# Optimization experiments

Measured on AMD Instinct MI355X. Metric: run time of the kernel, lower is better.

## Reference

```python
import jax, jax.numpy as jnp
import numpy as np

N, NV, NE = 256, 8192, 128


def setup_inputs() -> dict:
    key = jax.random.key(0)
    k1, k2, k3, k4 = jax.random.split(key, 4)
    return {
        "vertices": jax.random.normal(k1, (N, NV, NE), dtype=jnp.float32),
        "query": jax.random.normal(k2, (NE,), dtype=jnp.float32) * 0.003,
        "W_logit": jax.random.normal(k3, (NE,), dtype=jnp.float32) * (1.0 / np.sqrt(NE)),
        "b_logit": jnp.zeros((), dtype=jnp.float32),
        "W_reduce": jax.random.normal(k4, (NE, NE), dtype=jnp.float32) * (1.0 / np.sqrt(NE)),
        "b_reduce": jnp.zeros((NE,), dtype=jnp.float32),
        "temp": jnp.ones((), dtype=jnp.float32),
    }


def reference(vertices, query, W_logit, b_logit, W_reduce, b_reduce, temp):
    # vertices: [N, nV, nE]; query broadcasts as the single pooling query (nQ=1).
    # Additive tanh attention logits: fc_logit(tanh(context + query)) -> [N, nV]
    logits = jnp.tanh(vertices + query) @ W_logit + b_logit  # [N, nV]
    probs = jax.nn.softmax(logits / temp, axis=-1)            # softmax over vertices
    pooled = jnp.einsum("nv,nve->ne", probs, vertices)        # bmm(probs, memory)
    heads = jax.nn.leaky_relu(pooled)                          # default slope 0.01
    out = heads @ W_reduce.T + b_reduce                        # fc_reduceheads
    return out[:, None, :]  # [N, 1, nE]
```

## Files before the change

### kernel.cpp

```cpp
#include <hip/hip_runtime.h>
#include <math.h>

#define NN      256
#define NVV     8192
#define NEE     128
#define THREADS 1024
#define WAVES   (THREADS / 64)
#define SLICES  2
#define V_PER_BLOCK (NVV / SLICES)
#define GROUPS_PER_BLOCK (WAVES * 2)
#define V_PER_GROUP (V_PER_BLOCK / GROUPS_PER_BLOCK)

__global__ __launch_bounds__(THREADS, 2) void agp_main_kernel(
    const float* __restrict__ vertices,
    const float* __restrict__ query,
    const float* __restrict__ W_logit,
    const float* __restrict__ temp_p,
    float* __restrict__ pacc,
    float* __restrict__ pl)
{
    const int bid   = blockIdx.x;
    const int n     = bid >> 1;
    const int slice = bid & 1;
    const int tid   = threadIdx.x;
    const int wave  = tid >> 6;
    const int lane  = tid & 63;
    const int half  = lane >> 5;
    const int li    = lane & 31;
    const int e0    = li << 2;
    const int gid   = (wave << 1) | half;

    const float invT   = 1.0f / temp_p[0];
    const float ESCALE = invT * 1.4426950408889634f;
    const float C2L2E  = 2.8853900817779268f;

    const float4 q4  = *reinterpret_cast<const float4*>(query   + e0);
    const float4 wl4 = *reinterpret_cast<const float4*>(W_logit + e0);
    const float qc0 = q4.x * C2L2E, qc1 = q4.y * C2L2E;
    const float qc2 = q4.z * C2L2E, qc3 = q4.w * C2L2E;
    const float swl = wl4.x + wl4.y + wl4.z + wl4.w;

    const float* p = vertices
        + ((size_t)n * NVV + (size_t)slice * V_PER_BLOCK + gid) * NEE + e0;

    float a0 = 0.f, a1 = 0.f, a2 = 0.f, a3 = 0.f;
    float l  = 0.f;

    #pragma unroll 4
    for (int it = 0; it < V_PER_GROUP; ++it, p += GROUPS_PER_BLOCK * NEE) {
        const float4 x = *reinterpret_cast<const float4*>(p);

        float s2;
        s2 =      wl4.x * __builtin_amdgcn_rcpf(__builtin_amdgcn_exp2f(fmaf(x.x, C2L2E, qc0)) + 1.0f);
        s2 = fmaf(wl4.y,  __builtin_amdgcn_rcpf(__builtin_amdgcn_exp2f(fmaf(x.y, C2L2E, qc1)) + 1.0f), s2);
        s2 = fmaf(wl4.z,  __builtin_amdgcn_rcpf(__builtin_amdgcn_exp2f(fmaf(x.z, C2L2E, qc2)) + 1.0f), s2);
        s2 = fmaf(wl4.w,  __builtin_amdgcn_rcpf(__builtin_amdgcn_exp2f(fmaf(x.w, C2L2E, qc3)) + 1.0f), s2);
        float s = fmaf(-2.0f, s2, swl);

        s += __shfl_xor(s, 1);
        s += __shfl_xor(s, 2);
        s += __shfl_xor(s, 4);
        s += __shfl_xor(s, 8);
        s += __shfl_xor(s, 16);

        const float eb = __builtin_amdgcn_exp2f(s * ESCALE);
        l += eb;
        a0 = fmaf(eb, x.x, a0);
        a1 = fmaf(eb, x.y, a1);
        a2 = fmaf(eb, x.z, a2);
        a3 = fmaf(eb, x.w, a3);
    }

    __shared__ float sm_l[GROUPS_PER_BLOCK];
    __shared__ float sm_acc[GROUPS_PER_BLOCK][NEE];

    *reinterpret_cast<float4*>(&sm_acc[gid][e0]) = make_float4(a0, a1, a2, a3);
    if (li == 0) sm_l[gid] = l;
    __syncthreads();

    if (tid < NEE) {
        float L = 0.f, P = 0.f;
        #pragma unroll
        for (int g = 0; g < GROUPS_PER_BLOCK; ++g) {
            L += sm_l[g];
            P += sm_acc[g][tid];
        }
        pacc[(size_t)bid * NEE + tid] = P;
        if (tid == 0) pl[bid] = L;
    }
}

__global__ __launch_bounds__(NEE, 8) void agp_combine_kernel(
    const float* __restrict__ pacc,
    const float* __restrict__ pl,
    const float* __restrict__ W_reduce,
    const float* __restrict__ b_reduce,
    float* __restrict__ out)
{
    const int n   = blockIdx.x;
    const int tid = threadIdx.x;

    __shared__ float sm_heads[NEE];

    const float L = pl[n * SLICES + 0] + pl[n * SLICES + 1];
    float P = pacc[(size_t)(n * SLICES + 0) * NEE + tid]
            + pacc[(size_t)(n * SLICES + 1) * NEE + tid];
    float pooled = P / L;
    sm_heads[tid] = (pooled > 0.0f) ? pooled : 0.01f * pooled;
    __syncthreads();

    const float* wr = W_reduce + tid * NEE;
    float o = b_reduce[tid];
    #pragma unroll
    for (int k = 0; k < NEE; k += 4) {
        const float4 w = *reinterpret_cast<const float4*>(wr + k);
        o = fmaf(sm_heads[k + 0], w.x, o);
        o = fmaf(sm_heads[k + 1], w.y, o);
        o = fmaf(sm_heads[k + 2], w.z, o);
        o = fmaf(sm_heads[k + 3], w.w, o);
    }
    out[(size_t)n * NEE + tid] = o;
}

extern "C" void kernel_launch(void* const* d_in, const int* in_sizes, int n_in,
                              void* d_out, int out_size, void* d_ws, size_t ws_size,
                              hipStream_t stream) {
    const float* vertices = (const float*)d_in[0];
    const float* query    = (const float*)d_in[1];
    const float* W_logit  = (const float*)d_in[2];
    const float* W_reduce = (const float*)d_in[4];
    const float* b_reduce = (const float*)d_in[5];
    const float* temp_p   = (const float*)d_in[6];
    float* out = (float*)d_out;

    float* pacc = (float*)d_ws;
    float* pl   = pacc + (size_t)NN * SLICES * NEE;

    agp_main_kernel<<<NN * SLICES, THREADS, 0, stream>>>(
        vertices, query, W_logit, temp_p, pacc, pl);
    agp_combine_kernel<<<NN, NEE, 0, stream>>>(
        pacc, pl, W_reduce, b_reduce, out);
}
```

Before: 182.6 us.

## Fuse combine stage into main kernel via last-block atomic counter

Removes the separate combine kernel: each block publishes its partial sums, increments a per-row atomic counter, and the last block for each row finalizes normalization, leaky ReLU and the W_reduce matvec. The per-vertex logit math is also simplified by reducing the raw tanh term across lanes and folding the bias and scaling into one fma before exp2. This removes a dependent kernel launch but adds a memset launch, a fence and an atomic per block.

Result: slower. 440.7 us (+141.3%).

```diff
diff --git a/kernel.cpp b/kernel.cpp
--- a/kernel.cpp
+++ b/kernel.cpp
@@ -11,13 +11,17 @@
 #define GROUPS_PER_BLOCK (WAVES * 2)
 #define V_PER_GROUP (V_PER_BLOCK / GROUPS_PER_BLOCK)
 
-__global__ __launch_bounds__(THREADS, 2) void agp_main_kernel(
+__global__ __launch_bounds__(THREADS, 2) void agp_fused_kernel(
     const float* __restrict__ vertices,
     const float* __restrict__ query,
     const float* __restrict__ W_logit,
+    const float* __restrict__ W_reduce,
+    const float* __restrict__ b_reduce,
     const float* __restrict__ temp_p,
+    float* __restrict__ out,
     float* __restrict__ pacc,
-    float* __restrict__ pl)
+    float* __restrict__ pl,
+    unsigned int* __restrict__ cnt)
 {
     const int bid   = blockIdx.x;
     const int n     = bid >> 1;
@@ -38,7 +42,15 @@
     const float4 wl4 = *reinterpret_cast<const float4*>(W_logit + e0);
     const float qc0 = q4.x * C2L2E, qc1 = q4.y * C2L2E;
     const float qc2 = q4.z * C2L2E, qc3 = q4.w * C2L2E;
-    const float swl = wl4.x + wl4.y + wl4.z + wl4.w;
+
+    float swl = wl4.x + wl4.y + wl4.z + wl4.w;
+    swl += __shfl_xor(swl, 1);
+    swl += __shfl_xor(swl, 2);
+    swl += __shfl_xor(swl, 4);
+    swl += __shfl_xor(swl, 8);
+    swl += __shfl_xor(swl, 16);
+    const float A = swl * ESCALE;
+    const float B = -2.0f * ESCALE;
 
     const float* p = vertices
         + ((size_t)n * NVV + (size_t)slice * V_PER_BLOCK + gid) * NEE + e0;
@@ -55,15 +67,14 @@
         s2 = fmaf(wl4.y,  __builtin_amdgcn_rcpf(__builtin_amdgcn_exp2f(fmaf(x.y, C2L2E, qc1)) + 1.0f), s2);
         s2 = fmaf(wl4.z,  __builtin_amdgcn_rcpf(__builtin_amdgcn_exp2f(fmaf(x.z, C2L2E, qc2)) + 1.0f), s2);
         s2 = fmaf(wl4.w,  __builtin_amdgcn_rcpf(__builtin_amdgcn_exp2f(fmaf(x.w, C2L2E, qc3)) + 1.0f), s2);
-        float s = fmaf(-2.0f, s2, swl);
 
-        s += __shfl_xor(s, 1);
-        s += __shfl_xor(s, 2);
-        s += __shfl_xor(s, 4);
-        s += __shfl_xor(s, 8);
-        s += __shfl_xor(s, 16);
+        s2 += __shfl_xor(s2, 1);
+        s2 += __shfl_xor(s2, 2);
+        s2 += __shfl_xor(s2, 4);
+        s2 += __shfl_xor(s2, 8);
+        s2 += __shfl_xor(s2, 16);
 
-        const float eb = __builtin_amdgcn_exp2f(s * ESCALE);
+        const float eb = __builtin_amdgcn_exp2f(fmaf(B, s2, A));
         l += eb;
         a0 = fmaf(eb, x.x, a0);
         a1 = fmaf(eb, x.y, a1);
@@ -73,6 +84,8 @@
 
     __shared__ float sm_l[GROUPS_PER_BLOCK];
     __shared__ float sm_acc[GROUPS_PER_BLOCK][NEE];
+    __shared__ float sm_heads[NEE];
+    __shared__ int   sm_last;
 
     *reinterpret_cast<float4*>(&sm_acc[gid][e0]) = make_float4(a0, a1, a2, a3);
     if (li == 0) sm_l[gid] = l;
@@ -88,38 +101,39 @@
         pacc[(size_t)bid * NEE + tid] = P;
         if (tid == 0) pl[bid] = L;
     }
-}
-
-__global__ __launch_bounds__(NEE, 8) void agp_combine_kernel(
-    const float* __restrict__ pacc,
-    const float* __restrict__ pl,
-    const float* __restrict__ W_reduce,
-    const float* __restrict__ b_reduce,
-    float* __restrict__ out)
-{
-    const int n   = blockIdx.x;
-    const int tid = threadIdx.x;
-
-    __shared__ float sm_heads[NEE];
-
-    const float L = pl[n * SLICES + 0] + pl[n * SLICES + 1];
-    float P = pacc[(size_t)(n * SLICES + 0) * NEE + tid]
-            + pacc[(size_t)(n * SLICES + 1) * NEE + tid];
-    float pooled = P / L;
-    sm_heads[tid] = (pooled > 0.0f) ? pooled : 0.01f * pooled;
     __syncthreads();
 
-    const float* wr = W_reduce + tid * NEE;
-    float o = b_reduce[tid];
-    #pragma unroll
-    for (int k = 0; k < NEE; k += 4) {
-        const float4 w = *reinterpret_cast<const float4*>(wr + k);
-        o = fmaf(sm_heads[k + 0], w.x, o);
-        o = fmaf(sm_heads[k + 1], w.y, o);
-        o = fmaf(sm_heads[k + 2], w.z, o);
-        o = fmaf(sm_heads[k + 3], w.w, o);
+    if (tid == 0) {
+        __threadfence();
+        sm_last = (int)atomicAdd(&cnt[n], 1u);
     }
-    out[(size_t)n * NEE + tid] = o;
+    __syncthreads();
+    if (sm_last != SLICES - 1) return;
+
+    __threadfence();
+
+    if (tid < NEE) {
+        const float L = pl[n * SLICES + 0] + pl[n * SLICES + 1];
+        const float P = pacc[(size_t)(n * SLICES + 0) * NEE + tid]
+                      + pacc[(size_t)(n * SLICES + 1) * NEE + tid];
+        const float pooled = P / L;
+        sm_heads[tid] = (pooled > 0.0f) ? pooled : 0.01f * pooled;
+    }
+    __syncthreads();
+
+    if (tid < NEE) {
+        const float* wr = W_reduce + tid * NEE;
+        float o = b_reduce[tid];
+        #pragma unroll
+        for (int k = 0; k < NEE; k += 4) {
+            const float4 w = *reinterpret_cast<const float4*>(wr + k);
+            o = fmaf(sm_heads[k + 0], w.x, o);
+            o = fmaf(sm_heads[k + 1], w.y, o);
+            o = fmaf(sm_heads[k + 2], w.z, o);
+            o = fmaf(sm_heads[k + 3], w.w, o);
+        }
+        out[(size_t)n * NEE + tid] = o;
+    }
 }
 
 extern "C" void kernel_launch(void* const* d_in, const int* in_sizes, int n_in,
@@ -133,11 +147,13 @@
     const float* temp_p   = (const float*)d_in[6];
     float* out = (float*)d_out;
 
-    float* pacc = (float*)d_ws;
+    unsigned int* cnt = (unsigned int*)d_ws;
+    float* pacc = (float*)((char*)d_ws + NN * sizeof(unsigned int));
     float* pl   = pacc + (size_t)NN * SLICES * NEE;
 
-    agp_main_kernel<<<NN * SLICES, THREADS, 0, stream>>>(
-        vertices, query, W_logit, temp_p, pacc, pl);
-    agp_combine_kernel<<<NN, NEE, 0, stream>>>(
-        pacc, pl, W_reduce, b_reduce, out);
+    hipMemsetAsync(cnt, 0, NN * sizeof(unsigned int), stream);
+
+    agp_fused_kernel<<<NN * SLICES, THREADS, 0, stream>>>(
+        vertices, query, W_logit, W_reduce, b_reduce, temp_p, out,
+        pacc, pl, cnt);
 }
```
